# Kernel optimization log

Measured on AMD Instinct MI355X. Metric: run time of the kernel, lower is better.

## Reference

```python
import jax, jax.numpy as jnp
import numpy as np

EPS = float(np.finfo(np.float32).eps)  # matches torch.finfo(float32).eps
N_PTS, K_DIM, N_BINS = 1_000_000, 3, 21  # wv_tilde last dim = 2*N_BINS+1 = 43


def setup_inputs() -> dict:
    key = jax.random.key(0)
    k1, k2 = jax.random.split(key)
    # y in the open unit interval (points on the unit hypercube, per-coordinate)
    y = jax.random.uniform(k1, (N_PTS, K_DIM), jnp.float32, 1e-4, 1.0 - 1e-4)
    # network-predicted unnormalized widths/heights: [N, k, 2b+1]
    wv_tilde = jax.random.normal(k2, (N_PTS, K_DIM, 2 * N_BINS + 1), jnp.float32)
    return {"y": y, "wv_tilde": wv_tilde}


def _gather(t, idx):
    # gather along last axis with [..., 1] int index -> [...]
    return jnp.take_along_axis(t, idx, axis=-1)[..., 0]


def pwquad_flow(y, wv_tilde):
    """Faithful JAX port of ElementWisePWQuadraticTransform.flow (with jacobian)."""
    D = wv_tilde.shape[-1]
    nv = (D + 1) // 2                      # ceil(D/2) = b+1 vertex heights
    v_tilde = wv_tilde[..., :nv]           # [N,k,b+1]
    w_tilde = wv_tilde[..., nv:]           # [N,k,b]
    b = w_tilde.shape[-1]

    # normalized bin widths and their cumulative sums
    w = jnp.exp(w_tilde)
    wsum = jnp.cumsum(w, axis=-1)
    wnorm = wsum[..., -1:]
    w = w / wnorm
    wsum = wsum / wnorm
    zeros = jnp.zeros(wsum.shape[:-1] + (1,), wsum.dtype)
    wsum_shift = jnp.concatenate([zeros, wsum], axis=-1)   # [N,k,b+1]

    # modified softmax for vertex heights of the derivative (integrates to 1)
    ve = jnp.exp(v_tilde)
    trap = (ve[..., :-1] + ve[..., 1:]) * 0.5 * w          # trapezoid areas
    v = jnp.maximum(ve / trap.sum(-1, keepdims=True), 1e-6)  # [N,k,b+1]

    # cumulative CDF values at bin edges
    vw = jnp.concatenate(
        [zeros, jnp.cumsum((v[..., :-1] + v[..., 1:]) * 0.5 * w, axis=-1)],
        axis=-1)                                           # [N,k,b+1]

    # argmax-based bin search (identical to torch implementation)
    finder = jnp.where(vw > y[..., None], 0.0, 1.0)
    cat = jnp.concatenate([jnp.full_like(zeros, EPS), finder * (vw + 1.0)], axis=-1)
    mx = jnp.argmax(cat, axis=-1) - 1
    edges = jnp.clip(mx, 0, b - 1).astype(jnp.int32)[..., None]  # [N,k,1]

    v0 = _gather(v, edges)
    v1 = _gather(v, edges + 1)
    we = _gather(w, edges)

    # quadratic solve: (a/2) t^2 + bq t + c = 0  within the bin
    a = (v1 - v0) * we
    bq = v0 * we
    c = _gather(vw, edges) - y
    a = jnp.where(jnp.abs(a) < EPS, EPS, a)
    d = jnp.maximum(bq * bq - 2.0 * a * c, 0.0)
    sq = jnp.sqrt(d)
    sol1 = (-bq - sq) / a
    sol2 = (-bq + sq) / a
    sol = jnp.where((sol1 >= 0.0) & (sol1 < 1.0), sol1, sol2)
    sol = jnp.clip(sol, EPS, 1.0 - EPS)

    x = we * sol + _gather(wsum_shift, edges)
    x = jnp.clip(x, EPS, 1.0 - EPS)

    # log|det J| = -sum log(lerp(v0, v1, sol))
    logj = -jnp.sum(jnp.log(v0 + (v1 - v0) * sol), axis=-1, keepdims=True)
    return x, logj


def reference(y, wv_tilde):
    return pwquad_flow(y, wv_tilde)
```

## Files before the change

### kernel.cpp

```cpp
#include <hip/hip_runtime.h>
#include <math.h>

#define NROWS        3000000
#define ROWS_PER_BLK 192
#define NBINS        21
#define NV           22
#define DROW         43
#define FLOATS_PER_BLK (ROWS_PER_BLK * DROW)
#define F4_PER_BLK     (FLOATS_PER_BLK / 4)

__global__ __launch_bounds__(ROWS_PER_BLK) void pwquad_kernel(
    const float* __restrict__ y,
    const float* __restrict__ wv,
    float* __restrict__ out)
{
    __shared__ float lds[FLOATS_PER_BLK];
    __shared__ float lt[ROWS_PER_BLK];

    const int tid = threadIdx.x;
    const int blk = blockIdx.x;

    const float4* __restrict__ src4 =
        reinterpret_cast<const float4*>(wv + (long long)blk * FLOATS_PER_BLK);
    float4* l4 = reinterpret_cast<float4*>(lds);

    float4 r[10];
#pragma unroll
    for (int it = 0; it < 10; ++it) r[it] = src4[tid + it * ROWS_PER_BLK];
    const bool tail = (tid < (F4_PER_BLK - 10 * ROWS_PER_BLK));
    float4 rt;
    if (tail) rt = src4[tid + 10 * ROWS_PER_BLK];
#pragma unroll
    for (int it = 0; it < 10; ++it) l4[tid + it * ROWS_PER_BLK] = r[it];
    if (tail) l4[tid + 10 * ROWS_PER_BLK] = rt;
    __syncthreads();

    const int row = blk * ROWS_PER_BLK + tid;
    const float yv = y[row];
    const float* myrow = lds + tid * DROW;

    const float EPSF = 1.1920929e-07f;

    float w[NBINS];
    float wnorm = 0.f;
#pragma unroll
    for (int j = 0; j < NBINS; ++j) { w[j] = __expf(myrow[NV + j]); wnorm += w[j]; }
    const float invw = 1.0f / wnorm;
#pragma unroll
    for (int j = 0; j < NBINS; ++j) w[j] *= invw;

    float v[NV];
#pragma unroll
    for (int i = 0; i < NV; ++i) v[i] = __expf(myrow[i]);
    float T = 0.f;
#pragma unroll
    for (int j = 0; j < NBINS; ++j) T += (v[j] + v[j + 1]) * 0.5f * w[j];
    const float invT = 1.0f / T;
#pragma unroll
    for (int i = 0; i < NV; ++i) v[i] = fmaxf(v[i] * invT, 1e-6f);

    float vw = 0.f, wsum = 0.f;
    float vwe = 0.f, wse = 0.f;
    float v0 = v[0], v1 = v[1], we = w[0];
#pragma unroll
    for (int j = 0; j < 20; ++j) {
        const float inc = (v[j] + v[j + 1]) * 0.5f * w[j];
        vw += inc;
        wsum += w[j];
        const bool q = (vw <= yv);
        vwe = q ? vw       : vwe;
        wse = q ? wsum     : wse;
        v0  = q ? v[j + 1] : v0;
        v1  = q ? v[j + 2] : v1;
        we  = q ? w[j + 1] : we;
    }

    float a = (v1 - v0) * we;
    const float bq = v0 * we;
    const float c = vwe - yv;
    a = (fabsf(a) < EPSF) ? EPSF : a;
    const float dd = fmaxf(bq * bq - 2.0f * a * c, 0.f);
    const float sq = sqrtf(dd);
    const float sol1 = (-bq - sq) / a;
    const float sol2 = (-bq + sq) / a;
    float sol = (sol1 >= 0.f && sol1 < 1.f) ? sol1 : sol2;
    sol = fminf(fmaxf(sol, EPSF), 1.f - EPSF);
    float x = we * sol + wse;
    x = fminf(fmaxf(x, EPSF), 1.f - EPSF);
    out[row] = x;

    lt[tid] = __logf(v0 + (v1 - v0) * sol);
    __syncthreads();
    if (tid % 3 == 0) {
        out[NROWS + blk * (ROWS_PER_BLK / 3) + tid / 3] =
            -(lt[tid] + lt[tid + 1] + lt[tid + 2]);
    }
}

extern "C" void kernel_launch(void* const* d_in, const int* in_sizes, int n_in,
                              void* d_out, int out_size, void* d_ws, size_t ws_size,
                              hipStream_t stream) {
    const float* y  = (const float*)d_in[0];
    const float* wv = (const float*)d_in[1];
    float* out = (float*)d_out;

    const int nblocks = NROWS / ROWS_PER_BLK;
    pwquad_kernel<<<nblocks, ROWS_PER_BLK, 0, stream>>>(y, wv, out);
}
```

Measured before the change: 98.47 us.

## Make blocks persistent over five chunks with register-prefetched next chunk

Each block now handles five consecutive 192-row chunks instead of one. The global loads for the next chunk go into registers while the current chunk is computed out of LDS, which is meant to hide memory latency and cut the number of blocks launched. The cost is higher register pressure from keeping the float4 prefetch buffer live across the compute, plus fewer blocks in flight (3125), which may lower occupancy and the number of memory requests outstanding at once.

```diff
diff --git a/kernel.cpp b/kernel.cpp
--- a/kernel.cpp
+++ b/kernel.cpp
@@ -2,98 +2,115 @@
 #include <math.h>
 
 #define NROWS        3000000
-#define ROWS_PER_BLK 192
+#define ROWS_PER_CHK 192
+#define CHKS_PER_BLK 5
+#define NBLOCKS      3125
 #define NBINS        21
 #define NV           22
 #define DROW         43
-#define FLOATS_PER_BLK (ROWS_PER_BLK * DROW)
-#define F4_PER_BLK     (FLOATS_PER_BLK / 4)
+#define FLOATS_PER_CHK (ROWS_PER_CHK * DROW)
+#define F4_PER_CHK     (FLOATS_PER_CHK / 4)
+#define PTS_PER_CHK    (ROWS_PER_CHK / 3)
 
-__global__ __launch_bounds__(ROWS_PER_BLK) void pwquad_kernel(
+__global__ __launch_bounds__(ROWS_PER_CHK) void pwquad_kernel(
     const float* __restrict__ y,
     const float* __restrict__ wv,
     float* __restrict__ out)
 {
-    __shared__ float lds[FLOATS_PER_BLK];
-    __shared__ float lt[ROWS_PER_BLK];
+    __shared__ float lds[FLOATS_PER_CHK];
+    __shared__ float lt[ROWS_PER_CHK];
 
     const int tid = threadIdx.x;
-    const int blk = blockIdx.x;
-
-    const float4* __restrict__ src4 =
-        reinterpret_cast<const float4*>(wv + (long long)blk * FLOATS_PER_BLK);
+    const int c0  = blockIdx.x * CHKS_PER_BLK;
+    const float4* __restrict__ src4 = reinterpret_cast<const float4*>(wv);
     float4* l4 = reinterpret_cast<float4*>(lds);
-
-    float4 r[10];
-#pragma unroll
-    for (int it = 0; it < 10; ++it) r[it] = src4[tid + it * ROWS_PER_BLK];
-    const bool tail = (tid < (F4_PER_BLK - 10 * ROWS_PER_BLK));
-    float4 rt;
-    if (tail) rt = src4[tid + 10 * ROWS_PER_BLK];
-#pragma unroll
-    for (int it = 0; it < 10; ++it) l4[tid + it * ROWS_PER_BLK] = r[it];
-    if (tail) l4[tid + 10 * ROWS_PER_BLK] = rt;
-    __syncthreads();
-
-    const int row = blk * ROWS_PER_BLK + tid;
-    const float yv = y[row];
-    const float* myrow = lds + tid * DROW;
+    const bool tail = (tid < (F4_PER_CHK - 10 * ROWS_PER_CHK));
 
     const float EPSF = 1.1920929e-07f;
 
-    float w[NBINS];
-    float wnorm = 0.f;
+    float4 r[10], rt;
+    float yv_n;
+    {
+        const int base = c0 * F4_PER_CHK;
 #pragma unroll
-    for (int j = 0; j < NBINS; ++j) { w[j] = __expf(myrow[NV + j]); wnorm += w[j]; }
-    const float invw = 1.0f / wnorm;
-#pragma unroll
-    for (int j = 0; j < NBINS; ++j) w[j] *= invw;
-
-    float v[NV];
-#pragma unroll
-    for (int i = 0; i < NV; ++i) v[i] = __expf(myrow[i]);
-    float T = 0.f;
-#pragma unroll
-    for (int j = 0; j < NBINS; ++j) T += (v[j] + v[j + 1]) * 0.5f * w[j];
-    const float invT = 1.0f / T;
-#pragma unroll
-    for (int i = 0; i < NV; ++i) v[i] = fmaxf(v[i] * invT, 1e-6f);
-
-    float vw = 0.f, wsum = 0.f;
-    float vwe = 0.f, wse = 0.f;
-    float v0 = v[0], v1 = v[1], we = w[0];
-#pragma unroll
-    for (int j = 0; j < 20; ++j) {
-        const float inc = (v[j] + v[j + 1]) * 0.5f * w[j];
-        vw += inc;
-        wsum += w[j];
-        const bool q = (vw <= yv);
-        vwe = q ? vw       : vwe;
-        wse = q ? wsum     : wse;
-        v0  = q ? v[j + 1] : v0;
-        v1  = q ? v[j + 2] : v1;
-        we  = q ? w[j + 1] : we;
+        for (int it = 0; it < 10; ++it) r[it] = src4[base + tid + it * ROWS_PER_CHK];
+        if (tail) rt = src4[base + tid + 10 * ROWS_PER_CHK];
+        yv_n = y[c0 * ROWS_PER_CHK + tid];
     }
 
-    float a = (v1 - v0) * we;
-    const float bq = v0 * we;
-    const float c = vwe - yv;
-    a = (fabsf(a) < EPSF) ? EPSF : a;
-    const float dd = fmaxf(bq * bq - 2.0f * a * c, 0.f);
-    const float sq = sqrtf(dd);
-    const float sol1 = (-bq - sq) / a;
-    const float sol2 = (-bq + sq) / a;
-    float sol = (sol1 >= 0.f && sol1 < 1.f) ? sol1 : sol2;
-    sol = fminf(fmaxf(sol, EPSF), 1.f - EPSF);
-    float x = we * sol + wse;
-    x = fminf(fmaxf(x, EPSF), 1.f - EPSF);
-    out[row] = x;
+    for (int k = 0; k < CHKS_PER_BLK; ++k) {
+        const int c = c0 + k;
 
-    lt[tid] = __logf(v0 + (v1 - v0) * sol);
-    __syncthreads();
-    if (tid % 3 == 0) {
-        out[NROWS + blk * (ROWS_PER_BLK / 3) + tid / 3] =
-            -(lt[tid] + lt[tid + 1] + lt[tid + 2]);
+#pragma unroll
+        for (int it = 0; it < 10; ++it) l4[tid + it * ROWS_PER_CHK] = r[it];
+        if (tail) l4[tid + 10 * ROWS_PER_CHK] = rt;
+        const float yv = yv_n;
+        __syncthreads();
+
+        if (k + 1 < CHKS_PER_BLK) {
+            const int nb = (c + 1) * F4_PER_CHK;
+#pragma unroll
+            for (int it = 0; it < 10; ++it) r[it] = src4[nb + tid + it * ROWS_PER_CHK];
+            if (tail) rt = src4[nb + tid + 10 * ROWS_PER_CHK];
+            yv_n = y[(c + 1) * ROWS_PER_CHK + tid];
+        }
+
+        const float* myrow = lds + tid * DROW;
+
+        float w[NBINS];
+        float wnorm = 0.f;
+#pragma unroll
+        for (int j = 0; j < NBINS; ++j) { w[j] = __expf(myrow[NV + j]); wnorm += w[j]; }
+        const float invw = 1.0f / wnorm;
+#pragma unroll
+        for (int j = 0; j < NBINS; ++j) w[j] *= invw;
+
+        float v[NV];
+#pragma unroll
+        for (int i = 0; i < NV; ++i) v[i] = __expf(myrow[i]);
+        float T = 0.f;
+#pragma unroll
+        for (int j = 0; j < NBINS; ++j) T += (v[j] + v[j + 1]) * 0.5f * w[j];
+        const float invT = 1.0f / T;
+#pragma unroll
+        for (int i = 0; i < NV; ++i) v[i] = fmaxf(v[i] * invT, 1e-6f);
+
+        float vw = 0.f, wsum = 0.f;
+        float vwe = 0.f, wse = 0.f;
+        float v0 = v[0], v1 = v[1], we = w[0];
+#pragma unroll
+        for (int j = 0; j < 20; ++j) {
+            const float inc = (v[j] + v[j + 1]) * 0.5f * w[j];
+            vw += inc;
+            wsum += w[j];
+            const bool q = (vw <= yv);
+            vwe = q ? vw       : vwe;
+            wse = q ? wsum     : wse;
+            v0  = q ? v[j + 1] : v0;
+            v1  = q ? v[j + 2] : v1;
+            we  = q ? w[j + 1] : we;
+        }
+
+        float a = (v1 - v0) * we;
+        const float bq = v0 * we;
+        const float cc = vwe - yv;
+        a = (fabsf(a) < EPSF) ? EPSF : a;
+        const float dd = fmaxf(bq * bq - 2.0f * a * cc, 0.f);
+        const float sq = sqrtf(dd);
+        const float sol1 = (-bq - sq) / a;
+        const float sol2 = (-bq + sq) / a;
+        float sol = (sol1 >= 0.f && sol1 < 1.f) ? sol1 : sol2;
+        sol = fminf(fmaxf(sol, EPSF), 1.f - EPSF);
+        float x = we * sol + wse;
+        x = fminf(fmaxf(x, EPSF), 1.f - EPSF);
+        out[c * ROWS_PER_CHK + tid] = x;
+
+        lt[tid] = __logf(v0 + (v1 - v0) * sol);
+        __syncthreads();
+        if (tid % 3 == 0) {
+            out[NROWS + c * PTS_PER_CHK + tid / 3] =
+                -(lt[tid] + lt[tid + 1] + lt[tid + 2]);
+        }
     }
 }
 
@@ -104,6 +121,5 @@
     const float* wv = (const float*)d_in[1];
     float* out = (float*)d_out;
 
-    const int nblocks = NROWS / ROWS_PER_BLK;
-    pwquad_kernel<<<nblocks, ROWS_PER_BLK, 0, stream>>>(y, wv, out);
+    pwquad_kernel<<<NBLOCKS, ROWS_PER_CHK, 0, stream>>>(y, wv, out);
 }
```

Measured after the change: 215.7 us. 2.19x slower.

## Double-buffer persistent-block loop with direct global-to-LDS async loads

Applied to the files above, without the earlier changes.

Each block now loops over ten 96-row chunks, double-buffering the input in LDS with global_load_lds so the load of the next chunk can overlap compute on the current one. The y values are also staged through LDS. Only half the threads compute in each phase, which halves ALU utilisation per block, and the grid shrinks to about 3125 blocks. Each phase waits on vmcnt(0) before its barrier, which may serialize the prefetch and limit the overlap.

```diff
diff --git a/kernel.cpp b/kernel.cpp
--- a/kernel.cpp
+++ b/kernel.cpp
@@ -2,98 +2,127 @@
 #include <math.h>
 
 #define NROWS        3000000
-#define ROWS_PER_BLK 192
+#define NTHREADS     192
+#define HALF_ROWS    96
 #define NBINS        21
 #define NV           22
 #define DROW         43
-#define FLOATS_PER_BLK (ROWS_PER_BLK * DROW)
-#define F4_PER_BLK     (FLOATS_PER_BLK / 4)
+#define F_PER_HALF   (HALF_ROWS * DROW)
+#define F4_PER_HALF  (F_PER_HALF / 4)
+#define PHASES       10
+#define NBLOCKS      (NROWS / (HALF_ROWS * PHASES))
 
-__global__ __launch_bounds__(ROWS_PER_BLK) void pwquad_kernel(
+#define AS1 __attribute__((address_space(1)))
+#define AS3 __attribute__((address_space(3)))
+
+__device__ __forceinline__ void gload_lds16(const void* g, void* l) {
+    __builtin_amdgcn_global_load_lds((const AS1 void*)g, (AS3 void*)l, 16, 0, 0);
+}
+
+__device__ __forceinline__ void prefetch_half(const float* __restrict__ wv,
+                                              const float* __restrict__ y,
+                                              int hp, float* buf, float* yb, int tid)
+{
+    const float4* s4 = reinterpret_cast<const float4*>(wv) + (size_t)hp * F4_PER_HALF;
+    float4* d4 = reinterpret_cast<float4*>(buf);
+#pragma unroll
+    for (int it = 0; it < 5; ++it)
+        gload_lds16(s4 + it * NTHREADS + tid, d4 + it * NTHREADS + tid);
+    if (tid < (F4_PER_HALF - 5 * NTHREADS))
+        gload_lds16(s4 + 5 * NTHREADS + tid, d4 + 5 * NTHREADS + tid);
+    if (tid >= 128 && tid < 128 + (HALF_ROWS / 4)) {
+        const float4* ys = reinterpret_cast<const float4*>(y)
+                           + (size_t)hp * (HALF_ROWS / 4) + (tid - 128);
+        gload_lds16(ys, reinterpret_cast<float4*>(yb) + (tid - 128));
+    }
+}
+
+__global__ __launch_bounds__(NTHREADS) void pwquad_kernel(
     const float* __restrict__ y,
     const float* __restrict__ wv,
     float* __restrict__ out)
 {
-    __shared__ float lds[FLOATS_PER_BLK];
-    __shared__ float lt[ROWS_PER_BLK];
+    __shared__ float buf[2][F_PER_HALF];
+    __shared__ float yb[2][HALF_ROWS];
+    __shared__ float lt[2][HALF_ROWS];
 
     const int tid = threadIdx.x;
-    const int blk = blockIdx.x;
+    const int h0  = blockIdx.x * PHASES;
+    const float EPSF = 1.1920929e-07f;
 
-    const float4* __restrict__ src4 =
-        reinterpret_cast<const float4*>(wv + (long long)blk * FLOATS_PER_BLK);
-    float4* l4 = reinterpret_cast<float4*>(lds);
-
-    float4 r[10];
-#pragma unroll
-    for (int it = 0; it < 10; ++it) r[it] = src4[tid + it * ROWS_PER_BLK];
-    const bool tail = (tid < (F4_PER_BLK - 10 * ROWS_PER_BLK));
-    float4 rt;
-    if (tail) rt = src4[tid + 10 * ROWS_PER_BLK];
-#pragma unroll
-    for (int it = 0; it < 10; ++it) l4[tid + it * ROWS_PER_BLK] = r[it];
-    if (tail) l4[tid + 10 * ROWS_PER_BLK] = rt;
+    prefetch_half(wv, y, h0, buf[0], yb[0], tid);
+    asm volatile("s_waitcnt vmcnt(0) lgkmcnt(0)" ::: "memory");
     __syncthreads();
 
-    const int row = blk * ROWS_PER_BLK + tid;
-    const float yv = y[row];
-    const float* myrow = lds + tid * DROW;
+    for (int p = 0; p < PHASES; ++p) {
+        const int cur = p & 1;
+        const int hp  = h0 + p;
 
-    const float EPSF = 1.1920929e-07f;
+        if (p + 1 < PHASES)
+            prefetch_half(wv, y, hp + 1, buf[cur ^ 1], yb[cur ^ 1], tid);
 
-    float w[NBINS];
-    float wnorm = 0.f;
+        if (tid < HALF_ROWS) {
+            const float yv = yb[cur][tid];
+            const float* myrow = &buf[cur][tid * DROW];
+
+            float w[NBINS];
+            float wnorm = 0.f;
 #pragma unroll
-    for (int j = 0; j < NBINS; ++j) { w[j] = __expf(myrow[NV + j]); wnorm += w[j]; }
-    const float invw = 1.0f / wnorm;
+            for (int j = 0; j < NBINS; ++j) { w[j] = __expf(myrow[NV + j]); wnorm += w[j]; }
+            const float invw = 1.0f / wnorm;
 #pragma unroll
-    for (int j = 0; j < NBINS; ++j) w[j] *= invw;
+            for (int j = 0; j < NBINS; ++j) w[j] *= invw;
 
-    float v[NV];
+            float v[NV];
 #pragma unroll
-    for (int i = 0; i < NV; ++i) v[i] = __expf(myrow[i]);
-    float T = 0.f;
+            for (int i = 0; i < NV; ++i) v[i] = __expf(myrow[i]);
+            float T = 0.f;
 #pragma unroll
-    for (int j = 0; j < NBINS; ++j) T += (v[j] + v[j + 1]) * 0.5f * w[j];
-    const float invT = 1.0f / T;
+            for (int j = 0; j < NBINS; ++j) T += (v[j] + v[j + 1]) * 0.5f * w[j];
+            const float invT = 1.0f / T;
 #pragma unroll
-    for (int i = 0; i < NV; ++i) v[i] = fmaxf(v[i] * invT, 1e-6f);
+            for (int i = 0; i < NV; ++i) v[i] = fmaxf(v[i] * invT, 1e-6f);
 
-    float vw = 0.f, wsum = 0.f;
-    float vwe = 0.f, wse = 0.f;
-    float v0 = v[0], v1 = v[1], we = w[0];
+            float vw = 0.f, wsum = 0.f;
+            float vwe = 0.f, wse = 0.f;
+            float v0 = v[0], v1 = v[1], we = w[0];
 #pragma unroll
-    for (int j = 0; j < 20; ++j) {
-        const float inc = (v[j] + v[j + 1]) * 0.5f * w[j];
-        vw += inc;
-        wsum += w[j];
-        const bool q = (vw <= yv);
-        vwe = q ? vw       : vwe;
-        wse = q ? wsum     : wse;
-        v0  = q ? v[j + 1] : v0;
-        v1  = q ? v[j + 2] : v1;
-        we  = q ? w[j + 1] : we;
-    }
+            for (int j = 0; j < 20; ++j) {
+                const float inc = (v[j] + v[j + 1]) * 0.5f * w[j];
+                vw += inc;
+                wsum += w[j];
+                const bool q = (vw <= yv);
+                vwe = q ? vw       : vwe;
+                wse = q ? wsum     : wse;
+                v0  = q ? v[j + 1] : v0;
+                v1  = q ? v[j + 2] : v1;
+                we  = q ? w[j + 1] : we;
+            }
 
-    float a = (v1 - v0) * we;
-    const float bq = v0 * we;
-    const float c = vwe - yv;
-    a = (fabsf(a) < EPSF) ? EPSF : a;
-    const float dd = fmaxf(bq * bq - 2.0f * a * c, 0.f);
-    const float sq = sqrtf(dd);
-    const float sol1 = (-bq - sq) / a;
-    const float sol2 = (-bq + sq) / a;
-    float sol = (sol1 >= 0.f && sol1 < 1.f) ? sol1 : sol2;
-    sol = fminf(fmaxf(sol, EPSF), 1.f - EPSF);
-    float x = we * sol + wse;
-    x = fminf(fmaxf(x, EPSF), 1.f - EPSF);
-    out[row] = x;
+            float a = (v1 - v0) * we;
+            const float bq = v0 * we;
+            const float cc = vwe - yv;
+            a = (fabsf(a) < EPSF) ? EPSF : a;
+            const float dd = fmaxf(bq * bq - 2.0f * a * cc, 0.f);
+            const float sq = sqrtf(dd);
+            const float sol1 = (-bq - sq) / a;
+            const float sol2 = (-bq + sq) / a;
+            float sol = (sol1 >= 0.f && sol1 < 1.f) ? sol1 : sol2;
+            sol = fminf(fmaxf(sol, EPSF), 1.f - EPSF);
+            float x = we * sol + wse;
+            x = fminf(fmaxf(x, EPSF), 1.f - EPSF);
+            out[hp * HALF_ROWS + tid] = x;
 
-    lt[tid] = __logf(v0 + (v1 - v0) * sol);
-    __syncthreads();
-    if (tid % 3 == 0) {
-        out[NROWS + blk * (ROWS_PER_BLK / 3) + tid / 3] =
-            -(lt[tid] + lt[tid + 1] + lt[tid + 2]);
+            lt[cur][tid] = __logf(v0 + (v1 - v0) * sol);
+        }
+
+        asm volatile("s_waitcnt vmcnt(0) lgkmcnt(0)" ::: "memory");
+        __syncthreads();
+
+        if (tid < HALF_ROWS && (tid % 3) == 0) {
+            out[NROWS + hp * (HALF_ROWS / 3) + tid / 3] =
+                -(lt[cur][tid] + lt[cur][tid + 1] + lt[cur][tid + 2]);
+        }
     }
 }
 
@@ -104,6 +133,5 @@
     const float* wv = (const float*)d_in[1];
     float* out = (float*)d_out;
 
-    const int nblocks = NROWS / ROWS_PER_BLK;
-    pwquad_kernel<<<nblocks, ROWS_PER_BLK, 0, stream>>>(y, wv, out);
+    pwquad_kernel<<<NBLOCKS, NTHREADS, 0, stream>>>(y, wv, out);
 }
```

New measurement: 136.7 us. +38.8%, slower.

## Use direct global-to-LDS loads with one wavefront handling three rows per thread

Applied to the files above, without the earlier changes.

Each block becomes a single 64-thread wavefront that loads its 192-row tile of wv and y straight into LDS with global_load_lds, so the data no longer passes through registers. Each thread then processes the three coordinates of one point, summing the log-jacobian in registers. This removes the second __syncthreads and the LDS reduction for logj. In exchange each thread runs three times the serial work, and occupancy depends on the roughly 33 KB of LDS per single-wave block.

```diff
diff --git a/kernel.cpp b/kernel.cpp
--- a/kernel.cpp
+++ b/kernel.cpp
@@ -2,99 +2,108 @@
 #include <math.h>
 
 #define NROWS        3000000
+#define NPTS         1000000
+#define NTHREADS     64
 #define ROWS_PER_BLK 192
 #define NBINS        21
 #define NV           22
 #define DROW         43
-#define FLOATS_PER_BLK (ROWS_PER_BLK * DROW)
-#define F4_PER_BLK     (FLOATS_PER_BLK / 4)
+#define F_PER_BLK    (ROWS_PER_BLK * DROW)
+#define F4_PER_BLK   (F_PER_BLK / 4)
+#define NBLOCKS      (NROWS / ROWS_PER_BLK)
 
-__global__ __launch_bounds__(ROWS_PER_BLK) void pwquad_kernel(
+#define AS1 __attribute__((address_space(1)))
+#define AS3 __attribute__((address_space(3)))
+
+__device__ __forceinline__ void gload16(const void* g, void* l) {
+    __builtin_amdgcn_global_load_lds((const AS1 void*)g, (AS3 void*)l, 16, 0, 0);
+}
+
+__global__ __launch_bounds__(NTHREADS) void pwquad_kernel(
     const float* __restrict__ y,
     const float* __restrict__ wv,
     float* __restrict__ out)
 {
-    __shared__ float lds[FLOATS_PER_BLK];
-    __shared__ float lt[ROWS_PER_BLK];
+    __shared__ float buf[F_PER_BLK];
+    __shared__ float yb[ROWS_PER_BLK];
 
     const int tid = threadIdx.x;
-    const int blk = blockIdx.x;
-
-    const float4* __restrict__ src4 =
-        reinterpret_cast<const float4*>(wv + (long long)blk * FLOATS_PER_BLK);
-    float4* l4 = reinterpret_cast<float4*>(lds);
-
-    float4 r[10];
-#pragma unroll
-    for (int it = 0; it < 10; ++it) r[it] = src4[tid + it * ROWS_PER_BLK];
-    const bool tail = (tid < (F4_PER_BLK - 10 * ROWS_PER_BLK));
-    float4 rt;
-    if (tail) rt = src4[tid + 10 * ROWS_PER_BLK];
-#pragma unroll
-    for (int it = 0; it < 10; ++it) l4[tid + it * ROWS_PER_BLK] = r[it];
-    if (tail) l4[tid + 10 * ROWS_PER_BLK] = rt;
-    __syncthreads();
-
-    const int row = blk * ROWS_PER_BLK + tid;
-    const float yv = y[row];
-    const float* myrow = lds + tid * DROW;
-
+    const int b   = blockIdx.x;
     const float EPSF = 1.1920929e-07f;
 
-    float w[NBINS];
-    float wnorm = 0.f;
+    {
+        const float4* s = reinterpret_cast<const float4*>(wv) + (size_t)b * F4_PER_BLK;
+        float4* d = reinterpret_cast<float4*>(buf);
 #pragma unroll
-    for (int j = 0; j < NBINS; ++j) { w[j] = __expf(myrow[NV + j]); wnorm += w[j]; }
-    const float invw = 1.0f / wnorm;
+        for (int it = 0; it < 32; ++it)
+            gload16(s + it * NTHREADS + tid, d + it * NTHREADS + tid);
+        if (tid < 16)
+            gload16(s + 32 * NTHREADS + tid, d + 32 * NTHREADS + tid);
+        if (tid < 48)
+            gload16(reinterpret_cast<const float4*>(y) + (size_t)b * 48 + tid,
+                    reinterpret_cast<float4*>(yb) + tid);
+    }
+    asm volatile("s_waitcnt vmcnt(0)" ::: "memory");
+
+    float logj = 0.f;
+
+    for (int r = 0; r < 3; ++r) {
+        const int rrow = 3 * tid + r;
+        const float* myrow = &buf[rrow * DROW];
+        const float yv = yb[rrow];
+
+        float w[NBINS];
+        float wnorm = 0.f;
 #pragma unroll
-    for (int j = 0; j < NBINS; ++j) w[j] *= invw;
+        for (int j = 0; j < NBINS; ++j) { w[j] = __expf(myrow[NV + j]); wnorm += w[j]; }
+        const float invw = 1.0f / wnorm;
+#pragma unroll
+        for (int j = 0; j < NBINS; ++j) w[j] *= invw;
 
-    float v[NV];
+        float v[NV];
 #pragma unroll
-    for (int i = 0; i < NV; ++i) v[i] = __expf(myrow[i]);
-    float T = 0.f;
+        for (int i = 0; i < NV; ++i) v[i] = __expf(myrow[i]);
+        float T = 0.f;
 #pragma unroll
-    for (int j = 0; j < NBINS; ++j) T += (v[j] + v[j + 1]) * 0.5f * w[j];
-    const float invT = 1.0f / T;
+        for (int j = 0; j < NBINS; ++j) T += (v[j] + v[j + 1]) * 0.5f * w[j];
+        const float invT = 1.0f / T;
 #pragma unroll
-    for (int i = 0; i < NV; ++i) v[i] = fmaxf(v[i] * invT, 1e-6f);
+        for (int i = 0; i < NV; ++i) v[i] = fmaxf(v[i] * invT, 1e-6f);
 
-    float vw = 0.f, wsum = 0.f;
-    float vwe = 0.f, wse = 0.f;
-    float v0 = v[0], v1 = v[1], we = w[0];
+        float vw = 0.f, wsum = 0.f;
+        float vwe = 0.f, wse = 0.f;
+        float v0 = v[0], v1 = v[1], we = w[0];
 #pragma unroll
-    for (int j = 0; j < 20; ++j) {
-        const float inc = (v[j] + v[j + 1]) * 0.5f * w[j];
-        vw += inc;
-        wsum += w[j];
-        const bool q = (vw <= yv);
-        vwe = q ? vw       : vwe;
-        wse = q ? wsum     : wse;
-        v0  = q ? v[j + 1] : v0;
-        v1  = q ? v[j + 2] : v1;
-        we  = q ? w[j + 1] : we;
+        for (int j = 0; j < 20; ++j) {
+            const float inc = (v[j] + v[j + 1]) * 0.5f * w[j];
+            vw += inc;
+            wsum += w[j];
+            const bool q = (vw <= yv);
+            vwe = q ? vw       : vwe;
+            wse = q ? wsum     : wse;
+            v0  = q ? v[j + 1] : v0;
+            v1  = q ? v[j + 2] : v1;
+            we  = q ? w[j + 1] : we;
+        }
+
+        float a = (v1 - v0) * we;
+        const float bq = v0 * we;
+        const float cc = vwe - yv;
+        a = (fabsf(a) < EPSF) ? EPSF : a;
+        const float dd = fmaxf(bq * bq - 2.0f * a * cc, 0.f);
+        const float sq = sqrtf(dd);
+        const float sol1 = (-bq - sq) / a;
+        const float sol2 = (-bq + sq) / a;
+        float sol = (sol1 >= 0.f && sol1 < 1.f) ? sol1 : sol2;
+        sol = fminf(fmaxf(sol, EPSF), 1.f - EPSF);
+        float x = we * sol + wse;
+        x = fminf(fmaxf(x, EPSF), 1.f - EPSF);
+
+        out[(size_t)b * ROWS_PER_BLK + rrow] = x;
+        logj += __logf(v0 + (v1 - v0) * sol);
     }
 
-    float a = (v1 - v0) * we;
-    const float bq = v0 * we;
-    const float c = vwe - yv;
-    a = (fabsf(a) < EPSF) ? EPSF : a;
-    const float dd = fmaxf(bq * bq - 2.0f * a * c, 0.f);
-    const float sq = sqrtf(dd);
-    const float sol1 = (-bq - sq) / a;
-    const float sol2 = (-bq + sq) / a;
-    float sol = (sol1 >= 0.f && sol1 < 1.f) ? sol1 : sol2;
-    sol = fminf(fmaxf(sol, EPSF), 1.f - EPSF);
-    float x = we * sol + wse;
-    x = fminf(fmaxf(x, EPSF), 1.f - EPSF);
-    out[row] = x;
-
-    lt[tid] = __logf(v0 + (v1 - v0) * sol);
-    __syncthreads();
-    if (tid % 3 == 0) {
-        out[NROWS + blk * (ROWS_PER_BLK / 3) + tid / 3] =
-            -(lt[tid] + lt[tid + 1] + lt[tid + 2]);
-    }
+    out[NROWS + (size_t)b * NTHREADS + tid] = -logj;
 }
 
 extern "C" void kernel_launch(void* const* d_in, const int* in_sizes, int n_in,
@@ -104,6 +113,5 @@
     const float* wv = (const float*)d_in[1];
     float* out = (float*)d_out;
 
-    const int nblocks = NROWS / ROWS_PER_BLK;
-    pwquad_kernel<<<nblocks, ROWS_PER_BLK, 0, stream>>>(y, wv, out);
+    pwquad_kernel<<<NBLOCKS, NTHREADS, 0, stream>>>(y, wv, out);
 }
```

Result: slower. 122.0 us (+23.9%).
